# Optimization experiments

Measured on AMD Instinct MI355X. Metric: run time of the kernel, lower is better.

## Reference

```python
import jax, jax.numpy as jnp
import numpy as np

B, IN, H = 8192, 1024, 1024

def setup_inputs() -> dict:
    key = jax.random.key(0)
    ks = jax.random.split(key, 12)
    s_i = 1.0 / np.sqrt(IN)   # lecun-normal-ish scale for input kernels
    s_h = 1.0 / np.sqrt(H)
    d = {
        'inputs': jax.random.normal(ks[0], (B, IN), jnp.float32),
        'c': jax.random.normal(ks[1], (B, H), jnp.float32),
        'h': jax.random.normal(ks[2], (B, H), jnp.float32),
    }
    for n, k in zip(['Wii', 'Wif', 'Wig', 'Wio'], ks[3:7]):
        d[n] = jax.random.normal(k, (IN, H), jnp.float32) * s_i
    for n, k in zip(['Whi', 'Whf', 'Whg', 'Who'], ks[7:11]):
        d[n] = jax.random.normal(k, (H, H), jnp.float32) * s_h
    for n in ['bi', 'bf', 'bg', 'bo']:
        d[n] = jnp.zeros((H,), jnp.float32)
    return d

def reference(inputs, c, h, Wii, Wif, Wig, Wio, Whi, Whf, Whg, Who, bi, bf, bg, bo):
    # i = sigmoid(x Wii + h Whi + bi); f, o likewise; g = tanh(x Wig + h Whg + bg)
    i = jax.nn.sigmoid(inputs @ Wii + h @ Whi + bi)
    f = jax.nn.sigmoid(inputs @ Wif + h @ Whf + bf)
    g = jnp.tanh(inputs @ Wig + h @ Whg + bg)
    o = jax.nn.sigmoid(inputs @ Wio + h @ Who + bo)
    new_c = f * c + i * g
    new_h = o * jnp.tanh(new_c)
    return (new_c, new_h)
```

## Files before the change

kernel.cpp:

```cpp
#include <hip/hip_runtime.h>
#include <hip/hip_bf16.h>
#include <cstdint>


#define B_DIM 8192
#define H_DIM 1024
#define K2    2048
#define N4    4096
#define BK    64
#define BM    128
#define BN    256

typedef __bf16 bf16x8 __attribute__((ext_vector_type(8)));
typedef __bf16 bf16x4 __attribute__((ext_vector_type(4)));
typedef float  f32x4  __attribute__((ext_vector_type(4)));
typedef float  f32x16 __attribute__((ext_vector_type(16)));

__device__ __forceinline__ void async_load16(const __bf16* g, __bf16* l) {
  __builtin_amdgcn_global_load_lds(
      (__attribute__((address_space(1))) void*)(g),
      (__attribute__((address_space(3))) void*)(l),
      16, 0, 0);
}

__device__ __forceinline__ float sigm(float x) {
  return 1.0f / (1.0f + __expf(-x));
}
__device__ __forceinline__ float tanh_fast(float x) {
  return 2.0f / (1.0f + __expf(-2.0f * x)) - 1.0f;
}

__global__ void cast_a(const float* __restrict__ x, const float* __restrict__ h,
                       __bf16* __restrict__ A) {
  int row = blockIdx.x;
  int k = threadIdx.x << 3;
  const float* src = (k < H_DIM) ? (x + (size_t)row * H_DIM + k)
                                 : (h + (size_t)row * H_DIM + (k - H_DIM));
  float4 v0 = *(const float4*)src;
  float4 v1 = *(const float4*)(src + 4);
  bf16x8 o;
  o[0] = (__bf16)v0.x; o[1] = (__bf16)v0.y; o[2] = (__bf16)v0.z; o[3] = (__bf16)v0.w;
  o[4] = (__bf16)v1.x; o[5] = (__bf16)v1.y; o[6] = (__bf16)v1.z; o[7] = (__bf16)v1.w;
  *(bf16x8*)&A[(size_t)row * K2 + k] = o;
}

__global__ void cast_w(const float* __restrict__ Wii, const float* __restrict__ Wif,
                       const float* __restrict__ Wig, const float* __restrict__ Wio,
                       const float* __restrict__ Whi, const float* __restrict__ Whf,
                       const float* __restrict__ Whg, const float* __restrict__ Who,
                       __bf16* __restrict__ Bt) {
  __shared__ float tile[64][33];
  int k0 = blockIdx.x * 64;
  int j0 = blockIdx.y * 32;
  int gate = blockIdx.z;
  const float* Wi[4] = {Wii, Wif, Wig, Wio};
  const float* Wh[4] = {Whi, Whf, Whg, Who};
  const float* W = (k0 < H_DIM) ? Wi[gate] : Wh[gate];
  int kb = (k0 < H_DIM) ? k0 : (k0 - H_DIM);

  int col = threadIdx.x & 31;
  int rr  = threadIdx.x >> 5;
#pragma unroll
  for (int p = 0; p < 8; ++p)
    tile[p * 8 + rr][col] = W[(size_t)(kb + p * 8 + rr) * H_DIM + j0 + col];
  __syncthreads();

  int jj = threadIdx.x >> 3;
  int ko = threadIdx.x & 7;
  int j = j0 + jj;
  int p = ((j >> 5) << 7) + (gate << 5) + (j & 31);
  bf16x8 o;
#pragma unroll
  for (int t = 0; t < 8; ++t) o[t] = (__bf16)tile[ko * 8 + t][jj];
  *(bf16x8*)&Bt[(size_t)p * K2 + k0 + ko * 8] = o;
}

__global__ __launch_bounds__(256, 2) void lstm_gemm(
    const __bf16* __restrict__ A,
    const __bf16* __restrict__ Bt,
    const float* __restrict__ c,
    const float* __restrict__ bi, const float* __restrict__ bf_,
    const float* __restrict__ bg, const float* __restrict__ bo,
    float* __restrict__ out_c, float* __restrict__ out_h) {
  __shared__ __align__(16) __bf16 As[BM * BK];
  __shared__ __align__(16) __bf16 Bs[BN * BK];

  const int tid  = threadIdx.x;
  const int wave = tid >> 6;
  const int lane = tid & 63;
  const int wm   = wave >> 1;
  const int wn   = wave & 1;
  const int m0   = blockIdx.x * BM;
  const int n0   = blockIdx.y * BN;

  f32x16 acc[2][4] = {};

  const int l31 = lane & 31;
  const int h8  = lane >> 5;

  const int rin  = lane >> 3;
  const int slot = lane & 7;
  const int sg   = slot ^ rin;
  const __bf16* gA[4]; const __bf16* gB[8];
  __bf16* lA[4]; __bf16* lB[8];
#pragma unroll
  for (int cc = 0; cc < 4; ++cc) {
    int r = wave * 32 + cc * 8 + rin;
    gA[cc] = A + (size_t)(m0 + r) * K2 + sg * 8;
    lA[cc] = &As[(wave * 4 + cc) * 512];
  }
#pragma unroll
  for (int cc = 0; cc < 8; ++cc) {
    int r = wave * 64 + cc * 8 + rin;
    gB[cc] = Bt + (size_t)(n0 + r) * K2 + sg * 8;
    lB[cc] = &Bs[(wave * 8 + cc) * 512];
  }

  for (int k0 = 0; k0 < K2; k0 += BK) {
    __syncthreads();
#pragma unroll
    for (int cc = 0; cc < 4; ++cc) async_load16(gA[cc] + k0, lA[cc]);
#pragma unroll
    for (int cc = 0; cc < 8; ++cc) async_load16(gB[cc] + k0, lB[cc]);
    __syncthreads();

#pragma unroll
    for (int ks = 0; ks < 4; ++ks) {
      bf16x8 af[2], bfr[4];
      const int sw = ((ks * 2 + h8) ^ (l31 & 7)) * 8;
#pragma unroll
      for (int t = 0; t < 2; ++t)
        af[t] = *(const bf16x8*)&As[(wm * 64 + t * 32 + l31) * BK + sw];
#pragma unroll
      for (int t = 0; t < 4; ++t)
        bfr[t] = *(const bf16x8*)&Bs[(wn * 128 + t * 32 + l31) * BK + sw];

#pragma unroll
      for (int tm = 0; tm < 2; ++tm)
#pragma unroll
        for (int tn = 0; tn < 4; ++tn)
          acc[tm][tn] = __builtin_amdgcn_mfma_f32_32x32x16_bf16(
              af[tm], bfr[tn], acc[tm][tn], 0, 0, 0);
    }
  }

  const int j = blockIdx.y * 64 + wn * 32 + l31;
  const float vbi = bi[j], vbf = bf_[j], vbg = bg[j], vbo = bo[j];

#pragma unroll
  for (int tm = 0; tm < 2; ++tm) {
#pragma unroll
    for (int r = 0; r < 16; ++r) {
      int row = m0 + wm * 64 + tm * 32 + 4 * h8 + (r & 3) + 8 * (r >> 2);
      float gi = sigm(acc[tm][0][r] + vbi);
      float gf = sigm(acc[tm][1][r] + vbf);
      float gg = tanh_fast(acc[tm][2][r] + vbg);
      float go = sigm(acc[tm][3][r] + vbo);
      size_t idx = (size_t)row * H_DIM + j;
      float cv = c[idx];
      float nc = gf * cv + gi * gg;
      float nh = go * tanh_fast(nc);
      out_c[idx] = nc;
      out_h[idx] = nh;
    }
  }
}

extern "C" void kernel_launch(void* const* d_in, const int* in_sizes, int n_in,
                              void* d_out, int out_size, void* d_ws, size_t ws_size,
                              hipStream_t stream) {
  const float* x   = (const float*)d_in[0];
  const float* c   = (const float*)d_in[1];
  const float* h   = (const float*)d_in[2];
  const float* Wii = (const float*)d_in[3];
  const float* Wif = (const float*)d_in[4];
  const float* Wig = (const float*)d_in[5];
  const float* Wio = (const float*)d_in[6];
  const float* Whi = (const float*)d_in[7];
  const float* Whf = (const float*)d_in[8];
  const float* Whg = (const float*)d_in[9];
  const float* Who = (const float*)d_in[10];
  const float* bi  = (const float*)d_in[11];
  const float* bf_ = (const float*)d_in[12];
  const float* bg  = (const float*)d_in[13];
  const float* bo  = (const float*)d_in[14];

  __bf16* Abf = (__bf16*)d_ws;
  __bf16* Bt  = (__bf16*)((char*)d_ws + (size_t)B_DIM * K2 * 2);

  float* out_c = (float*)d_out;
  float* out_h = out_c + (size_t)B_DIM * H_DIM;

  cast_a<<<B_DIM, 256, 0, stream>>>(x, h, Abf);
  dim3 gw(K2 / 64, H_DIM / 32, 4);
  cast_w<<<gw, 256, 0, stream>>>(Wii, Wif, Wig, Wio, Whi, Whf, Whg, Who, Bt);
  dim3 gg(B_DIM / BM, N4 / BN);
  lstm_gemm<<<gg, 256, 0, stream>>>(Abf, Bt, c, bi, bf_, bg, bo, out_c, out_h);
}
```

Measured before the change: 347.7 us.

## Pre-pack weights in MFMA fragment layout, load B from global, double-buffer A

The weight cast kernel now writes B in a layout that matches the MFMA operand fragments, so each lane can read its B operand straight from global memory with one contiguous 16-byte load. The B tile no longer goes through LDS. A is double-buffered in LDS and the next tile is prefetched while the current one is used, which drops one barrier per iteration. The cost is that B reads now come from global/L2 inside the inner loop and are not shared between the two waves that use the same columns, so more global traffic and latency lands in the MFMA loop.

After: 361.7 us. 4.0% more time.

```diff
diff --git a/kernel.cpp b/kernel.cpp
--- a/kernel.cpp
+++ b/kernel.cpp
@@ -12,8 +12,6 @@
 #define BN    256
 
 typedef __bf16 bf16x8 __attribute__((ext_vector_type(8)));
-typedef __bf16 bf16x4 __attribute__((ext_vector_type(4)));
-typedef float  f32x4  __attribute__((ext_vector_type(4)));
 typedef float  f32x16 __attribute__((ext_vector_type(16)));
 
 __device__ __forceinline__ void async_load16(const __bf16* g, __bf16* l) {
@@ -48,10 +46,11 @@
                        const float* __restrict__ Wig, const float* __restrict__ Wio,
                        const float* __restrict__ Whi, const float* __restrict__ Whf,
                        const float* __restrict__ Whg, const float* __restrict__ Who,
-                       __bf16* __restrict__ Bt) {
+                       __bf16* __restrict__ Bt2) {
   __shared__ float tile[64][33];
   int k0 = blockIdx.x * 64;
-  int j0 = blockIdx.y * 32;
+  int jg = blockIdx.y;
+  int j0 = jg * 32;
   int gate = blockIdx.z;
   const float* Wi[4] = {Wii, Wif, Wig, Wio};
   const float* Wh[4] = {Whi, Whf, Whg, Who};
@@ -65,25 +64,25 @@
     tile[p * 8 + rr][col] = W[(size_t)(kb + p * 8 + rr) * H_DIM + j0 + col];
   __syncthreads();
 
-  int jj = threadIdx.x >> 3;
-  int ko = threadIdx.x & 7;
-  int j = j0 + jj;
-  int p = ((j >> 5) << 7) + (gate << 5) + (j & 31);
+  int jj = threadIdx.x & 31;
+  int kq = threadIdx.x >> 5;
+  int kt = (k0 >> 4) + (kq >> 1);
+  int h8 = kq & 1;
   bf16x8 o;
 #pragma unroll
-  for (int t = 0; t < 8; ++t) o[t] = (__bf16)tile[ko * 8 + t][jj];
-  *(bf16x8*)&Bt[(size_t)p * K2 + k0 + ko * 8] = o;
+  for (int e = 0; e < 8; ++e) o[e] = (__bf16)tile[kq * 8 + e][jj];
+  size_t chunk = ((size_t)jg * 128 + kt) * 4 + gate;
+  *(bf16x8*)&Bt2[chunk * 512 + (h8 * 32 + jj) * 8] = o;
 }
 
 __global__ __launch_bounds__(256, 2) void lstm_gemm(
     const __bf16* __restrict__ A,
-    const __bf16* __restrict__ Bt,
+    const __bf16* __restrict__ Bt2,
     const float* __restrict__ c,
     const float* __restrict__ bi, const float* __restrict__ bf_,
     const float* __restrict__ bg, const float* __restrict__ bo,
     float* __restrict__ out_c, float* __restrict__ out_h) {
-  __shared__ __align__(16) __bf16 As[BM * BK];
-  __shared__ __align__(16) __bf16 Bs[BN * BK];
+  __shared__ __align__(16) __bf16 As[2][BM * BK];
 
   const int tid  = threadIdx.x;
   const int wave = tid >> 6;
@@ -91,7 +90,7 @@
   const int wm   = wave >> 1;
   const int wn   = wave & 1;
   const int m0   = blockIdx.x * BM;
-  const int n0   = blockIdx.y * BN;
+  const int jg   = blockIdx.y * 2 + wn;
 
   f32x16 acc[2][4] = {};
 
@@ -101,50 +100,54 @@
   const int rin  = lane >> 3;
   const int slot = lane & 7;
   const int sg   = slot ^ rin;
-  const __bf16* gA[4]; const __bf16* gB[8];
-  __bf16* lA[4]; __bf16* lB[8];
+  const __bf16* gA[4];
+  int lA[4];
 #pragma unroll
   for (int cc = 0; cc < 4; ++cc) {
     int r = wave * 32 + cc * 8 + rin;
     gA[cc] = A + (size_t)(m0 + r) * K2 + sg * 8;
-    lA[cc] = &As[(wave * 4 + cc) * 512];
+    lA[cc] = (wave * 4 + cc) * 512;
   }
-#pragma unroll
-  for (int cc = 0; cc < 8; ++cc) {
-    int r = wave * 64 + cc * 8 + rin;
-    gB[cc] = Bt + (size_t)(n0 + r) * K2 + sg * 8;
-    lB[cc] = &Bs[(wave * 8 + cc) * 512];
-  }
-
-  for (int k0 = 0; k0 < K2; k0 += BK) {
+
+  const __bf16* bbase = Bt2 + ((size_t)jg * 128 * 4) * 512 + lane * 8;
+
+#pragma unroll
+  for (int cc = 0; cc < 4; ++cc) async_load16(gA[cc], &As[0][lA[cc]]);
+
+  for (int it = 0; it < K2 / BK; ++it) {
+    const int k0 = it * BK;
+    const int p  = it & 1;
     __syncthreads();
-#pragma unroll
-    for (int cc = 0; cc < 4; ++cc) async_load16(gA[cc] + k0, lA[cc]);
-#pragma unroll
-    for (int cc = 0; cc < 8; ++cc) async_load16(gB[cc] + k0, lB[cc]);
-    __syncthreads();
-
+    if (it + 1 < K2 / BK) {
+#pragma unroll
+      for (int cc = 0; cc < 4; ++cc)
+        async_load16(gA[cc] + k0 + BK, &As[p ^ 1][lA[cc]]);
+    }
+
+    const int kt0 = k0 >> 4;
 #pragma unroll
     for (int ks = 0; ks < 4; ++ks) {
-      bf16x8 af[2], bfr[4];
+      bf16x8 bfr[4];
+#pragma unroll
+      for (int g = 0; g < 4; ++g)
+        bfr[g] = *(const bf16x8*)(bbase + ((size_t)(kt0 + ks) * 4 + g) * 512);
+
+      bf16x8 af[2];
       const int sw = ((ks * 2 + h8) ^ (l31 & 7)) * 8;
 #pragma unroll
       for (int t = 0; t < 2; ++t)
-        af[t] = *(const bf16x8*)&As[(wm * 64 + t * 32 + l31) * BK + sw];
-#pragma unroll
-      for (int t = 0; t < 4; ++t)
-        bfr[t] = *(const bf16x8*)&Bs[(wn * 128 + t * 32 + l31) * BK + sw];
+        af[t] = *(const bf16x8*)&As[p][(wm * 64 + t * 32 + l31) * BK + sw];
 
 #pragma unroll
       for (int tm = 0; tm < 2; ++tm)
 #pragma unroll
-        for (int tn = 0; tn < 4; ++tn)
-          acc[tm][tn] = __builtin_amdgcn_mfma_f32_32x32x16_bf16(
-              af[tm], bfr[tn], acc[tm][tn], 0, 0, 0);
+        for (int g = 0; g < 4; ++g)
+          acc[tm][g] = __builtin_amdgcn_mfma_f32_32x32x16_bf16(
+              af[tm], bfr[g], acc[tm][g], 0, 0, 0);
     }
   }
 
-  const int j = blockIdx.y * 64 + wn * 32 + l31;
+  const int j = jg * 32 + l31;
   const float vbi = bi[j], vbf = bf_[j], vbg = bg[j], vbo = bo[j];
 
 #pragma unroll
@@ -186,14 +189,14 @@
   const float* bo  = (const float*)d_in[14];
 
   __bf16* Abf = (__bf16*)d_ws;
-  __bf16* Bt  = (__bf16*)((char*)d_ws + (size_t)B_DIM * K2 * 2);
+  __bf16* Bt2 = (__bf16*)((char*)d_ws + (size_t)B_DIM * K2 * 2);
 
   float* out_c = (float*)d_out;
   float* out_h = out_c + (size_t)B_DIM * H_DIM;
 
   cast_a<<<B_DIM, 256, 0, stream>>>(x, h, Abf);
   dim3 gw(K2 / 64, H_DIM / 32, 4);
-  cast_w<<<gw, 256, 0, stream>>>(Wii, Wif, Wig, Wio, Whi, Whf, Whg, Who, Bt);
+  cast_w<<<gw, 256, 0, stream>>>(Wii, Wif, Wig, Wio, Whi, Whf, Whg, Who, Bt2);
   dim3 gg(B_DIM / BM, N4 / BN);
-  lstm_gemm<<<gg, 256, 0, stream>>>(Abf, Bt, c, bi, bf_, bg, bo, out_c, out_h);
-}
+  lstm_gemm<<<gg, 256, 0, stream>>>(Abf, Bt2, c, bi, bf_, bg, bo, out_c, out_h);
+}
```
